# Optimization experiments

Hardware: AMD Instinct MI355X
Metric: run time of the kernel (lower is better)

The kernel has to match this reference:

```python
import jax, jax.numpy as jnp
import numpy as np

EPS = 1e-5


def setup_inputs() -> dict:
    key = jax.random.key(0)
    ks = jax.random.split(key, 8)
    g, p, d, h, w = 32, 64, 512, 24, 8
    hw = h * w
    return {
        "gal_fea": jax.random.normal(ks[0], (g, d, h, w), dtype=jnp.float32),
        "prob_fea": jax.random.normal(ks[1], (p, d, h, w), dtype=jnp.float32),
        "bn_weight": jnp.ones((1,), jnp.float32),
        "bn_bias": jnp.zeros((1,), jnp.float32),
        "bn_mean": jax.random.normal(ks[2], (1,), jnp.float32) * 0.1,
        "bn_var": jax.random.uniform(ks[3], (1,), jnp.float32, 0.5, 1.5),
        "fc_weight": jax.random.normal(ks[4], (1, 2 * hw), jnp.float32) * 0.05,
        "fc_bias": jnp.zeros((1,), jnp.float32),
        "lbn_weight": jnp.ones((1,), jnp.float32),
        "lbn_bias": jnp.zeros((1,), jnp.float32),
        "lbn_mean": jax.random.normal(ks[5], (1,), jnp.float32) * 0.1,
        "lbn_var": jax.random.uniform(ks[6], (1,), jnp.float32, 0.5, 1.5),
    }


def reference(gal_fea, prob_fea, bn_weight, bn_bias, bn_mean, bn_var,
              fc_weight, fc_bias, lbn_weight, lbn_bias, lbn_mean, lbn_var):
    g, d, h, w = gal_fea.shape
    p = prob_fea.shape[0]
    hw = h * w
    # 1x1 conv with probe pixels as kernels == batched correlation (QK^T style)
    gal = gal_fea.reshape(g, d, hw)                                  # [g, d, hw_x]
    ker = jnp.transpose(prob_fea, (0, 2, 3, 1)).reshape(p, hw, d)    # [p, hw_y, d]
    s = jnp.einsum('gdx,pyd->gpyx', gal, ker)                        # [g, p, hw_y, hw_x]
    # dual-axis max pooling, then concat: [g, p, 2*hw]
    score = jnp.concatenate([s.max(axis=2), s.max(axis=3)], axis=-1)
    # BatchNorm1d(1) in eval mode: scalar affine with running stats
    score = (score - bn_mean) * (bn_weight / jnp.sqrt(bn_var + EPS)) + bn_bias
    # fc: Linear(2*hw, 1)
    score = score.reshape(g * p, 2 * hw) @ fc_weight[0] + fc_bias[0]  # [g*p]
    score = score.reshape(g, p)
    # logit BatchNorm1d(1), eval mode
    score = (score - lbn_mean) * (lbn_weight / jnp.sqrt(lbn_var + EPS)) + lbn_bias
    return jax.nn.sigmoid(score / 10.0)
```

## Files before the change

kernel.cpp:

```cpp
#include <hip/hip_runtime.h>
#include <hip/hip_bf16.h>
#include <cstdint>
#include <cstddef>

#define NG 32
#define NP 64
#define ND 512
#define HW 192
#define KS 32
#define EPSV 1e-5f

typedef _Float16 half8 __attribute__((ext_vector_type(8)));
typedef float floatx4 __attribute__((ext_vector_type(4)));
typedef float floatx16 __attribute__((ext_vector_type(16)));

__global__ __launch_bounds__(256) void prep_frag(const float* __restrict__ gal,
                                                 const float* __restrict__ prob,
                                                 _Float16* __restrict__ galT4,
                                                 _Float16* __restrict__ probT4) {
  __shared__ float lds[16 * 192];
  const int z = blockIdx.x;
  const int ks = blockIdx.y;
  const float* src;
  _Float16* dst;
  if (z < NP) {
    src = prob + (size_t)z * ND * HW;
    dst = probT4 + (size_t)z * 98304;
  } else {
    src = gal + (size_t)(z - NP) * ND * HW;
    dst = galT4 + (size_t)(z - NP) * 98304;
  }
  src += (size_t)ks * 16 * HW;
  dst += (size_t)ks * 3072;
  const int t = threadIdx.x;
#pragma unroll
  for (int i = 0; i < 12; ++i) lds[i * 256 + t] = src[i * 256 + t];
  __syncthreads();
#pragma unroll
  for (int r = 0; r < 2; ++r) {
    const int h = r * 256 + t;
    if (h < 384) {
      const int rb = h >> 6, hi = (h >> 5) & 1, l31 = h & 31;
      half8 v;
#pragma unroll
      for (int j = 0; j < 8; ++j) v[j] = (_Float16)lds[(hi * 8 + j) * 192 + rb * 32 + l31];
      *(half8*)(dst + (size_t)h * 8) = v;
    }
  }
}

__device__ __forceinline__ void g2l16(const void* g, void* l) {
  __builtin_amdgcn_global_load_lds(
      (const __attribute__((address_space(1))) void*)g,
      (__attribute__((address_space(3))) void*)l, 16, 0, 0);
}

__global__ __launch_bounds__(256, 2) void qaconv_main(
    const _Float16* __restrict__ galT4, const _Float16* __restrict__ probT4,
    const float* __restrict__ bn_w, const float* __restrict__ bn_b,
    const float* __restrict__ bn_m, const float* __restrict__ bn_v,
    const float* __restrict__ fc_w, const float* __restrict__ fc_b,
    const float* __restrict__ lbn_w, const float* __restrict__ lbn_b,
    const float* __restrict__ lbn_m, const float* __restrict__ lbn_v,
    float* __restrict__ out) {
  __shared__ __align__(16) char shmem[73728];
  __shared__ float colp[2][HW];
  __shared__ float wsum[4];
  float(*rowbuf)[66] = (float(*)[66])shmem;

  const int bid = blockIdx.x;
  const int g = bid >> 6, p = bid & 63;

  const int t = threadIdx.x;
  const int lane = t & 63, wid = t >> 6;
  const int wr = wid & 1;
  const int wc = wid >> 1;
  const int l31 = lane & 31, hi = lane >> 5;

  const _Float16* pAl = probT4 + (size_t)p * 98304 + wid * 512 + lane * 8;
  const _Float16* pBl = galT4 + (size_t)g * 98304 + wid * 512 + lane * 8;
  const int sdst = wid * 1024;

  char* const b0 = shmem;
  char* const b1 = shmem + 24576;
  char* const b2 = shmem + 49152;

  floatx16 acc[3][3];
#pragma unroll
  for (int ii = 0; ii < 3; ++ii)
#pragma unroll
    for (int jj = 0; jj < 3; ++jj) acc[ii][jj] = (floatx16)0.f;

  half8 raf[3], rbf[3];

#define STAGE(kt_, base_)                                            \
  {                                                                  \
    char* db_ = (base_) + sdst;                                      \
    const _Float16* sa_ = pAl + (size_t)(kt_)*6144;                  \
    const _Float16* sb_ = pBl + (size_t)(kt_)*6144;                  \
    g2l16(sa_, db_);                                                 \
    g2l16(sa_ + 2048, db_ + 4096);                                   \
    g2l16(sa_ + 4096, db_ + 8192);                                   \
    g2l16(sb_, db_ + 12288);                                         \
    g2l16(sb_ + 2048, db_ + 16384);                                  \
    g2l16(sb_ + 4096, db_ + 20480);                                  \
  }

#define READ6(base_, kc_)                                            \
  {                                                                  \
    const char* bA_ = (base_) + (kc_)*6144;                          \
    const char* bB_ = (base_) + 12288 + (kc_)*6144;                  \
    raf[0] = *(const half8*)(bA_ + (wr * 3 + 0) * 1024 + lane * 16); \
    raf[1] = *(const half8*)(bA_ + (wr * 3 + 1) * 1024 + lane * 16); \
    raf[2] = *(const half8*)(bA_ + (wr * 3 + 2) * 1024 + lane * 16); \
    rbf[0] = *(const half8*)(bB_ + (wc * 3 + 0) * 1024 + lane * 16); \
    rbf[1] = *(const half8*)(bB_ + (wc * 3 + 1) * 1024 + lane * 16); \
    rbf[2] = *(const half8*)(bB_ + (wc * 3 + 2) * 1024 + lane * 16); \
  }

#define MFMA9()                                                                  \
  {                                                                              \
    __builtin_amdgcn_s_setprio(1);                                               \
    _Pragma("unroll") for (int ii = 0; ii < 3; ++ii)                             \
        _Pragma("unroll") for (int jj = 0; jj < 3; ++jj)                         \
            acc[ii][jj] = __builtin_amdgcn_mfma_f32_32x32x16_f16(raf[ii], rbf[jj],\
                                                                 acc[ii][jj], 0, 0, 0); \
    __builtin_amdgcn_s_setprio(0);                                               \
  }

#define SLOT(kt_, rdb_, stb_, doStage_, vmW_)                        \
  {                                                                  \
                                                        \
    READ6(rdb_, 0)                                                   \
    if (doStage_) STAGE((kt_) + 2, stb_)                             \
    __builtin_amdgcn_sched_barrier(0);                               \
    __builtin_amdgcn_s_barrier();                                    \
    asm volatile("s_waitcnt lgkmcnt(0)" ::: "memory");               \
    __builtin_amdgcn_sched_barrier(0);                               \
    MFMA9()                                                          \
    __builtin_amdgcn_s_barrier();                                    \
                                                        \
    READ6(rdb_, 1)                                                   \
    __builtin_amdgcn_sched_barrier(0);                               \
    asm volatile("s_waitcnt vmcnt(" #vmW_ ")" ::: "memory");         \
    __builtin_amdgcn_s_barrier();                                    \
    asm volatile("s_waitcnt lgkmcnt(0)" ::: "memory");               \
    __builtin_amdgcn_sched_barrier(0);                               \
    MFMA9()                                                          \
    __builtin_amdgcn_s_barrier();                                    \
  }

  STAGE(0, b0)
  STAGE(1, b1)
  asm volatile("s_waitcnt vmcnt(6)" ::: "memory");
  __builtin_amdgcn_s_barrier();

#pragma unroll 1
  for (int m = 0; m < 4; ++m) {
    SLOT(3 * m + 0, b0, b2, true, 6)
    SLOT(3 * m + 1, b1, b0, true, 6)
    SLOT(3 * m + 2, b2, b1, true, 6)
  }
  SLOT(12, b0, b2, true, 6)
  SLOT(13, b1, b0, true, 6)
  SLOT(14, b2, b1, false, 0)
  SLOT(15, b0, b1, false, 0)
#undef STAGE
#undef READ6
#undef MFMA9
#undef SLOT

#pragma unroll
  for (int fb = 0; fb < 3; ++fb) {
    float v = -3.4e38f;
#pragma unroll
    for (int fa = 0; fa < 3; ++fa)
#pragma unroll
      for (int e = 0; e < 16; ++e) v = fmaxf(v, acc[fa][fb][e]);
    v = fmaxf(v, __shfl_xor(v, 32));
    if (lane < 32) colp[wr][wc * 96 + fb * 32 + lane] = v;
  }
  __syncthreads();
#pragma unroll
  for (int fa = 0; fa < 3; ++fa)
#pragma unroll
    for (int e = 0; e < 16; ++e) {
      float rv = acc[fa][0][e];
      rv = fmaxf(rv, acc[fa][1][e]);
      rv = fmaxf(rv, acc[fa][2][e]);
      const int Y = wr * 96 + fa * 32 + (e & 3) + 8 * (e >> 2) + 4 * hi;
      rowbuf[Y][wc * 32 + l31] = rv;
    }
  __syncthreads();

  float partial = 0.f;
  if (t < HW) {
    const float* rb = rowbuf[t];
    float rmax = -3.4e38f;
#pragma unroll
    for (int j = 0; j < 16; ++j) {
      const floatx4 v = *(const floatx4*)&rb[j * 4];
      rmax = fmaxf(rmax, fmaxf(fmaxf(v[0], v[1]), fmaxf(v[2], v[3])));
    }
    const float cmax = fmaxf(colp[0][t], colp[1][t]);
    const float scale = bn_w[0] / sqrtf(bn_v[0] + EPSV);
    const float bm = bn_m[0], bb = bn_b[0];
    partial = ((cmax - bm) * scale + bb) * fc_w[t] +
              ((rmax - bm) * scale + bb) * fc_w[HW + t];
  }
#pragma unroll
  for (int off = 1; off < 64; off <<= 1) partial += __shfl_xor(partial, off);
  if (lane == 0) wsum[wid] = partial;
  __syncthreads();
  if (t == 0) {
    const float sum = fc_b[0] + wsum[0] + wsum[1] + wsum[2] + wsum[3];
    const float logit = (sum - lbn_m[0]) * (lbn_w[0] / sqrtf(lbn_v[0] + EPSV)) + lbn_b[0];
    out[bid] = 1.f / (1.f + expf(-logit * 0.1f));
  }
}

__global__ __launch_bounds__(256) void qaconv_naive(
    const float* __restrict__ gal, const float* __restrict__ prob,
    const float* __restrict__ bn_w, const float* __restrict__ bn_b,
    const float* __restrict__ bn_m, const float* __restrict__ bn_v,
    const float* __restrict__ fc_w, const float* __restrict__ fc_b,
    const float* __restrict__ lbn_w, const float* __restrict__ lbn_b,
    const float* __restrict__ lbn_m, const float* __restrict__ lbn_v,
    float* __restrict__ out) {
  __shared__ float prow[ND];
  __shared__ float rowmaxs[HW];
  __shared__ float colmaxs[HW];
  __shared__ float red[4];
  const int bid = blockIdx.x;
  const int g = bid >> 6, p = bid & 63;
  const int t = threadIdx.x, lane = t & 63, wid = t >> 6;
  const float* gp = gal + (size_t)g * ND * HW;
  const float* pp = prob + (size_t)p * ND * HW;
  float colmax = -3.4e38f;
  for (int y = 0; y < HW; ++y) {
    for (int k = t; k < ND; k += 256) prow[k] = pp[(size_t)k * HW + y];
    __syncthreads();
    float sv = -3.4e38f;
    if (t < HW) {
      sv = 0.f;
      for (int k = 0; k < ND; ++k) sv = fmaf(prow[k], gp[(size_t)k * HW + t], sv);
      colmax = fmaxf(colmax, sv);
    }
    float m = sv;
#pragma unroll
    for (int off = 1; off < 64; off <<= 1) m = fmaxf(m, __shfl_xor(m, off));
    if (lane == 0) red[wid] = m;
    __syncthreads();
    if (t == 0) rowmaxs[y] = fmaxf(fmaxf(red[0], red[1]), fmaxf(red[2], red[3]));
    __syncthreads();
  }
  if (t < HW) colmaxs[t] = colmax;
  __syncthreads();
  float partial = 0.f;
  for (int j = t; j < 2 * HW; j += 256) {
    const float v = (j < HW) ? colmaxs[j] : rowmaxs[j - HW];
    const float sc = (v - bn_m[0]) * (bn_w[0] / sqrtf(bn_v[0] + EPSV)) + bn_b[0];
    partial += sc * fc_w[j];
  }
#pragma unroll
  for (int off = 1; off < 64; off <<= 1) partial += __shfl_xor(partial, off);
  if (lane == 0) red[wid] = partial;
  __syncthreads();
  if (t == 0) {
    const float sum = fc_b[0] + red[0] + red[1] + red[2] + red[3];
    const float logit = (sum - lbn_m[0]) * (lbn_w[0] / sqrtf(lbn_v[0] + EPSV)) + lbn_b[0];
    out[bid] = 1.f / (1.f + expf(-logit * 0.1f));
  }
}

extern "C" void kernel_launch(void* const* d_in, const int* in_sizes, int n_in,
                              void* d_out, int out_size, void* d_ws, size_t ws_size,
                              hipStream_t stream) {
  const float* gal = (const float*)d_in[0];
  const float* prob = (const float*)d_in[1];
  const float* bn_w = (const float*)d_in[2];
  const float* bn_b = (const float*)d_in[3];
  const float* bn_m = (const float*)d_in[4];
  const float* bn_v = (const float*)d_in[5];
  const float* fc_w = (const float*)d_in[6];
  const float* fc_b = (const float*)d_in[7];
  const float* lbn_w = (const float*)d_in[8];
  const float* lbn_b = (const float*)d_in[9];
  const float* lbn_m = (const float*)d_in[10];
  const float* lbn_v = (const float*)d_in[11];
  float* out = (float*)d_out;

  const size_t probT4_elems = (size_t)NP * 98304;
  const size_t galT4_elems = (size_t)NG * 98304;
  const size_t ws_needed = (probT4_elems + galT4_elems) * sizeof(_Float16);
  if (ws_size >= ws_needed) {
    _Float16* probT4 = (_Float16*)d_ws;
    _Float16* galT4 = probT4 + probT4_elems;
    prep_frag<<<dim3(NP + NG, KS), dim3(256), 0, stream>>>(gal, prob, galT4, probT4);
    qaconv_main<<<dim3(NG * NP), dim3(256), 0, stream>>>(
        galT4, probT4, bn_w, bn_b, bn_m, bn_v, fc_w, fc_b, lbn_w, lbn_b, lbn_m, lbn_v, out);
  } else {
    qaconv_naive<<<dim3(NG * NP), dim3(256), 0, stream>>>(
        gal, prob, bn_w, bn_b, bn_m, bn_v, fc_w, fc_b, lbn_w, lbn_b, lbn_m, lbn_v, out);
  }
}
```

Measured before the change: 89.88 us.

## Double-buffer MFMA register fragments to overlap LDS reads with matrix math

```diff
diff --git a/kernel.cpp b/kernel.cpp
--- a/kernel.cpp
+++ b/kernel.cpp
@@ -91,7 +91,7 @@
 #pragma unroll
     for (int jj = 0; jj < 3; ++jj) acc[ii][jj] = (floatx16)0.f;
 
-  half8 raf[3], rbf[3];
+  half8 raf0[3], rbf0[3], raf1[3], rbf1[3];
 
 #define STAGE(kt_, base_)                                            \
   {                                                                  \
@@ -106,47 +106,39 @@
     g2l16(sb_ + 4096, db_ + 20480);                                  \
   }
 
-#define READ6(base_, kc_)                                            \
+#define READ6(AF, BF, base_, kc_)                                    \
   {                                                                  \
     const char* bA_ = (base_) + (kc_)*6144;                          \
     const char* bB_ = (base_) + 12288 + (kc_)*6144;                  \
-    raf[0] = *(const half8*)(bA_ + (wr * 3 + 0) * 1024 + lane * 16); \
-    raf[1] = *(const half8*)(bA_ + (wr * 3 + 1) * 1024 + lane * 16); \
-    raf[2] = *(const half8*)(bA_ + (wr * 3 + 2) * 1024 + lane * 16); \
-    rbf[0] = *(const half8*)(bB_ + (wc * 3 + 0) * 1024 + lane * 16); \
-    rbf[1] = *(const half8*)(bB_ + (wc * 3 + 1) * 1024 + lane * 16); \
-    rbf[2] = *(const half8*)(bB_ + (wc * 3 + 2) * 1024 + lane * 16); \
-  }
-
-#define MFMA9()                                                                  \
+    AF[0] = *(const half8*)(bA_ + (wr * 3 + 0) * 1024 + lane * 16);  \
+    AF[1] = *(const half8*)(bA_ + (wr * 3 + 1) * 1024 + lane * 16);  \
+    AF[2] = *(const half8*)(bA_ + (wr * 3 + 2) * 1024 + lane * 16);  \
+    BF[0] = *(const half8*)(bB_ + (wc * 3 + 0) * 1024 + lane * 16);  \
+    BF[1] = *(const half8*)(bB_ + (wc * 3 + 1) * 1024 + lane * 16);  \
+    BF[2] = *(const half8*)(bB_ + (wc * 3 + 2) * 1024 + lane * 16);  \
+  }
+
+#define MFMA9(AF, BF)                                                            \
   {                                                                              \
     __builtin_amdgcn_s_setprio(1);                                               \
     _Pragma("unroll") for (int ii = 0; ii < 3; ++ii)                             \
         _Pragma("unroll") for (int jj = 0; jj < 3; ++jj)                         \
-            acc[ii][jj] = __builtin_amdgcn_mfma_f32_32x32x16_f16(raf[ii], rbf[jj],\
+            acc[ii][jj] = __builtin_amdgcn_mfma_f32_32x32x16_f16(AF[ii], BF[jj], \
                                                                  acc[ii][jj], 0, 0, 0); \
     __builtin_amdgcn_s_setprio(0);                                               \
   }
 
-#define SLOT(kt_, rdb_, stb_, doStage_, vmW_)                        \
+#define SLOT(kt_, rdb_, nrdb_, stb_, doStage_, vmW_)                 \
   {                                                                  \
-                                                        \
-    READ6(rdb_, 0)                                                   \
+         \
     if (doStage_) STAGE((kt_) + 2, stb_)                             \
-    __builtin_amdgcn_sched_barrier(0);                               \
+    READ6(raf1, rbf1, rdb_, 1)                                       \
+    MFMA9(raf0, rbf0)                                                \
     __builtin_amdgcn_s_barrier();                                    \
-    asm volatile("s_waitcnt lgkmcnt(0)" ::: "memory");               \
-    __builtin_amdgcn_sched_barrier(0);                               \
-    MFMA9()                                                          \
-    __builtin_amdgcn_s_barrier();                                    \
-                                                        \
-    READ6(rdb_, 1)                                                   \
-    __builtin_amdgcn_sched_barrier(0);                               \
+                 \
     asm volatile("s_waitcnt vmcnt(" #vmW_ ")" ::: "memory");         \
-    __builtin_amdgcn_s_barrier();                                    \
-    asm volatile("s_waitcnt lgkmcnt(0)" ::: "memory");               \
-    __builtin_amdgcn_sched_barrier(0);                               \
-    MFMA9()                                                          \
+    READ6(raf0, rbf0, nrdb_, 0)                                      \
+    MFMA9(raf1, rbf1)                                                \
     __builtin_amdgcn_s_barrier();                                    \
   }
 
@@ -154,17 +146,20 @@
   STAGE(1, b1)
   asm volatile("s_waitcnt vmcnt(6)" ::: "memory");
   __builtin_amdgcn_s_barrier();
+  READ6(raf0, rbf0, b0, 0)
 
 #pragma unroll 1
   for (int m = 0; m < 4; ++m) {
-    SLOT(3 * m + 0, b0, b2, true, 6)
-    SLOT(3 * m + 1, b1, b0, true, 6)
-    SLOT(3 * m + 2, b2, b1, true, 6)
-  }
-  SLOT(12, b0, b2, true, 6)
-  SLOT(13, b1, b0, true, 6)
-  SLOT(14, b2, b1, false, 0)
-  SLOT(15, b0, b1, false, 0)
+    SLOT(3 * m + 0, b0, b1, b2, true, 6)
+    SLOT(3 * m + 1, b1, b2, b0, true, 6)
+    SLOT(3 * m + 2, b2, b0, b1, true, 6)
+  }
+  SLOT(12, b0, b1, b2, true, 6)
+  SLOT(13, b1, b2, b0, true, 6)
+  SLOT(14, b2, b0, b1, false, 0)
+  READ6(raf1, rbf1, b0, 1)
+  MFMA9(raf0, rbf0)
+  MFMA9(raf1, rbf1)
 #undef STAGE
 #undef READ6
 #undef MFMA9
```

Measured after the change: 91.95 us. 2.3% more time.

## Process four probes per block with pipeline continuing across pairs

Applied to the files above, without the earlier changes.

```diff
diff --git a/kernel.cpp b/kernel.cpp
--- a/kernel.cpp
+++ b/kernel.cpp
@@ -63,13 +63,14 @@
     const float* __restrict__ lbn_w, const float* __restrict__ lbn_b,
     const float* __restrict__ lbn_m, const float* __restrict__ lbn_v,
     float* __restrict__ out) {
-  __shared__ __align__(16) char shmem[73728];
+  __shared__ __align__(16) char tiles[3][24576];
   __shared__ float colp[2][HW];
+  __shared__ float rowp[2][HW];
   __shared__ float wsum[4];
-  float(*rowbuf)[66] = (float(*)[66])shmem;
 
   const int bid = blockIdx.x;
-  const int g = bid >> 6, p = bid & 63;
+  const int g = bid >> 4;
+  const int p0 = (bid & 15) * 4;
 
   const int t = threadIdx.x;
   const int lane = t & 63, wid = t >> 6;
@@ -77,27 +78,30 @@
   const int wc = wid >> 1;
   const int l31 = lane & 31, hi = lane >> 5;
 
-  const _Float16* pAl = probT4 + (size_t)p * 98304 + wid * 512 + lane * 8;
-  const _Float16* pBl = galT4 + (size_t)g * 98304 + wid * 512 + lane * 8;
-  const int sdst = wid * 1024;
-
-  char* const b0 = shmem;
-  char* const b1 = shmem + 24576;
-  char* const b2 = shmem + 49152;
+  const float scale = bn_w[0] / sqrtf(bn_v[0] + EPSV);
+  const float bm = bn_m[0], bb = bn_b[0];
+  const float lscale = lbn_w[0] / sqrtf(lbn_v[0] + EPSV);
+  const float lm = lbn_m[0], lb = lbn_b[0];
+  const float fcb = fc_b[0];
+
+  const _Float16* pB = galT4 + (size_t)g * 98304 + (size_t)t * 8;
+  const _Float16* pA0 = probT4 + (size_t)p0 * 98304 + (size_t)t * 8;
+  const _Float16* pA1 = pA0 + 98304;
+  const _Float16* pA2 = pA1 + 98304;
+  const _Float16* pA3 = pA2 + 98304;
+
+  char* const T0 = tiles[0];
+  char* const T1 = tiles[1];
+  char* const T2 = tiles[2];
 
   floatx16 acc[3][3];
-#pragma unroll
-  for (int ii = 0; ii < 3; ++ii)
-#pragma unroll
-    for (int jj = 0; jj < 3; ++jj) acc[ii][jj] = (floatx16)0.f;
-
   half8 raf[3], rbf[3];
 
-#define STAGE(kt_, base_)                                            \
+#define STAGE(sA_, kt_, base_)                                       \
   {                                                                  \
-    char* db_ = (base_) + sdst;                                      \
-    const _Float16* sa_ = pAl + (size_t)(kt_)*6144;                  \
-    const _Float16* sb_ = pBl + (size_t)(kt_)*6144;                  \
+    char* db_ = (char*)(base_) + t * 16;                             \
+    const _Float16* sa_ = (sA_) + (size_t)(kt_)*6144;                \
+    const _Float16* sb_ = pB + (size_t)(kt_)*6144;                   \
     g2l16(sa_, db_);                                                 \
     g2l16(sa_ + 2048, db_ + 4096);                                   \
     g2l16(sa_ + 4096, db_ + 8192);                                   \
@@ -108,8 +112,8 @@
 
 #define READ6(base_, kc_)                                            \
   {                                                                  \
-    const char* bA_ = (base_) + (kc_)*6144;                          \
-    const char* bB_ = (base_) + 12288 + (kc_)*6144;                  \
+    const char* bA_ = (const char*)(base_) + (kc_)*6144;             \
+    const char* bB_ = (const char*)(base_) + 12288 + (kc_)*6144;     \
     raf[0] = *(const half8*)(bA_ + (wr * 3 + 0) * 1024 + lane * 16); \
     raf[1] = *(const half8*)(bA_ + (wr * 3 + 1) * 1024 + lane * 16); \
     raf[2] = *(const half8*)(bA_ + (wr * 3 + 2) * 1024 + lane * 16); \
@@ -128,95 +132,120 @@
     __builtin_amdgcn_s_setprio(0);                                               \
   }
 
-#define SLOT(kt_, rdb_, stb_, doStage_, vmW_)                        \
-  {                                                                  \
-                                                        \
-    READ6(rdb_, 0)                                                   \
-    if (doStage_) STAGE((kt_) + 2, stb_)                             \
-    __builtin_amdgcn_sched_barrier(0);                               \
-    __builtin_amdgcn_s_barrier();                                    \
-    asm volatile("s_waitcnt lgkmcnt(0)" ::: "memory");               \
-    __builtin_amdgcn_sched_barrier(0);                               \
-    MFMA9()                                                          \
-    __builtin_amdgcn_s_barrier();                                    \
-                                                        \
-    READ6(rdb_, 1)                                                   \
-    __builtin_amdgcn_sched_barrier(0);                               \
-    asm volatile("s_waitcnt vmcnt(" #vmW_ ")" ::: "memory");         \
-    __builtin_amdgcn_s_barrier();                                    \
-    asm volatile("s_waitcnt lgkmcnt(0)" ::: "memory");               \
-    __builtin_amdgcn_sched_barrier(0);                               \
-    MFMA9()                                                          \
-    __builtin_amdgcn_s_barrier();                                    \
-  }
-
-  STAGE(0, b0)
-  STAGE(1, b1)
-  asm volatile("s_waitcnt vmcnt(6)" ::: "memory");
+#define SLOT(rdb_, stb_, sA_, skt_, doStage_, vmW_)          \
+  {                                                          \
+    READ6(rdb_, 0)                                           \
+    if (doStage_) STAGE(sA_, skt_, stb_)                     \
+    __builtin_amdgcn_sched_barrier(0);                       \
+    __builtin_amdgcn_s_barrier();                            \
+    asm volatile("s_waitcnt lgkmcnt(0)" ::: "memory");       \
+    __builtin_amdgcn_sched_barrier(0);                       \
+    MFMA9()                                                  \
+    __builtin_amdgcn_s_barrier();                            \
+    READ6(rdb_, 1)                                           \
+    __builtin_amdgcn_sched_barrier(0);                       \
+    asm volatile("s_waitcnt vmcnt(" #vmW_ ")" ::: "memory"); \
+    __builtin_amdgcn_s_barrier();                            \
+    asm volatile("s_waitcnt lgkmcnt(0)" ::: "memory");       \
+    __builtin_amdgcn_sched_barrier(0);                       \
+    MFMA9()                                                  \
+    __builtin_amdgcn_s_barrier();                            \
+  }
+
+#define EPI(pidx_)                                                               \
+  {                                                                              \
+    _Pragma("unroll") for (int fb = 0; fb < 3; ++fb) {                           \
+      float v = -3.4e38f;                                                        \
+      _Pragma("unroll") for (int fa = 0; fa < 3; ++fa)                           \
+          _Pragma("unroll") for (int e = 0; e < 16; ++e)                         \
+              v = fmaxf(v, acc[fa][fb][e]);                                      \
+      v = fmaxf(v, __shfl_xor(v, 32));                                           \
+      if (lane < 32) colp[wr][wc * 96 + fb * 32 + lane] = v;                     \
+    }                                                                            \
+    _Pragma("unroll") for (int fa = 0; fa < 3; ++fa)                             \
+        _Pragma("unroll") for (int e = 0; e < 16; ++e) {                         \
+      float rv = fmaxf(fmaxf(acc[fa][0][e], acc[fa][1][e]), acc[fa][2][e]);      \
+      rv = fmaxf(rv, __shfl_xor(rv, 1));                                         \
+      rv = fmaxf(rv, __shfl_xor(rv, 2));                                         \
+      rv = fmaxf(rv, __shfl_xor(rv, 4));                                         \
+      rv = fmaxf(rv, __shfl_xor(rv, 8));                                         \
+      rv = fmaxf(rv, __shfl_xor(rv, 16));                                        \
+      if (l31 == 0) {                                                            \
+        const int Y = wr * 96 + fa * 32 + (e & 3) + 8 * (e >> 2) + 4 * hi;       \
+        rowp[wc][Y] = rv;                                                        \
+      }                                                                          \
+    }                                                                            \
+    asm volatile("s_waitcnt lgkmcnt(0)" ::: "memory");                           \
+    __builtin_amdgcn_s_barrier();                                                \
+    float partial = 0.f;                                                         \
+    if (t < HW) {                                                                \
+      const float rmax = fmaxf(rowp[0][t], rowp[1][t]);                          \
+      const float cmax = fmaxf(colp[0][t], colp[1][t]);                          \
+      partial = ((cmax - bm) * scale + bb) * fc_w[t] +                           \
+                ((rmax - bm) * scale + bb) * fc_w[HW + t];                       \
+    }                                                                            \
+    _Pragma("unroll") for (int off = 1; off < 64; off <<= 1)                     \
+        partial += __shfl_xor(partial, off);                                     \
+    if (lane == 0) wsum[wid] = partial;                                          \
+    asm volatile("s_waitcnt lgkmcnt(0)" ::: "memory");                           \
+    __builtin_amdgcn_s_barrier();                                                \
+    if (t == 0) {                                                                \
+      const float sum = fcb + wsum[0] + wsum[1] + wsum[2] + wsum[3];             \
+      const float logit = (sum - lm) * lscale + lb;                              \
+      out[pidx_] = 1.f / (1.f + expf(-logit * 0.1f));                            \
+    }                                                                            \
+  }
+
+#define ZACC()                                         \
+  _Pragma("unroll") for (int ii = 0; ii < 3; ++ii)     \
+      _Pragma("unroll") for (int jj = 0; jj < 3; ++jj) \
+          acc[ii][jj] = (floatx16)0.f;
+
+#define PAIRBODY(X0_, X1_, X2_, curA_, nxtA_, pidx_)   \
+  ZACC()                                               \
+  _Pragma("unroll 1") for (int m = 0; m < 4; ++m) {    \
+    SLOT(X0_, X2_, curA_, 3 * m + 2, 1, 3)             \
+    SLOT(X1_, X0_, curA_, 3 * m + 3, 1, 3)             \
+    SLOT(X2_, X1_, curA_, 3 * m + 4, 1, 3)             \
+  }                                                    \
+  SLOT(X0_, X2_, curA_, 14, 1, 3)                      \
+  SLOT(X1_, X0_, curA_, 15, 1, 3)                      \
+  SLOT(X2_, X1_, nxtA_, 0, 1, 3)                       \
+  SLOT(X0_, X2_, nxtA_, 1, 1, 3)                       \
+  EPI(pidx_)
+
+#define PAIRLAST(X0_, X1_, X2_, curA_, pidx_)          \
+  ZACC()                                               \
+  _Pragma("unroll 1") for (int m = 0; m < 4; ++m) {    \
+    SLOT(X0_, X2_, curA_, 3 * m + 2, 1, 3)             \
+    SLOT(X1_, X0_, curA_, 3 * m + 3, 1, 3)             \
+    SLOT(X2_, X1_, curA_, 3 * m + 4, 1, 3)             \
+  }                                                    \
+  SLOT(X0_, X2_, curA_, 14, 1, 3)                      \
+  SLOT(X1_, X0_, curA_, 15, 1, 3)                      \
+  SLOT(X2_, X1_, curA_, 0, 0, 0)                       \
+  SLOT(X0_, X2_, curA_, 0, 0, 0)                       \
+  EPI(pidx_)
+
+  STAGE(pA0, 0, T0)
+  STAGE(pA0, 1, T1)
+  asm volatile("s_waitcnt vmcnt(3)" ::: "memory");
   __builtin_amdgcn_s_barrier();
 
-#pragma unroll 1
-  for (int m = 0; m < 4; ++m) {
-    SLOT(3 * m + 0, b0, b2, true, 6)
-    SLOT(3 * m + 1, b1, b0, true, 6)
-    SLOT(3 * m + 2, b2, b1, true, 6)
-  }
-  SLOT(12, b0, b2, true, 6)
-  SLOT(13, b1, b0, true, 6)
-  SLOT(14, b2, b1, false, 0)
-  SLOT(15, b0, b1, false, 0)
+  const int pidx0 = bid * 4;
+  PAIRBODY(T0, T1, T2, pA0, pA1, pidx0 + 0)
+  PAIRBODY(T1, T2, T0, pA1, pA2, pidx0 + 1)
+  PAIRBODY(T2, T0, T1, pA2, pA3, pidx0 + 2)
+  PAIRLAST(T0, T1, T2, pA3, pidx0 + 3)
+
 #undef STAGE
 #undef READ6
 #undef MFMA9
 #undef SLOT
-
-#pragma unroll
-  for (int fb = 0; fb < 3; ++fb) {
-    float v = -3.4e38f;
-#pragma unroll
-    for (int fa = 0; fa < 3; ++fa)
-#pragma unroll
-      for (int e = 0; e < 16; ++e) v = fmaxf(v, acc[fa][fb][e]);
-    v = fmaxf(v, __shfl_xor(v, 32));
-    if (lane < 32) colp[wr][wc * 96 + fb * 32 + lane] = v;
-  }
-  __syncthreads();
-#pragma unroll
-  for (int fa = 0; fa < 3; ++fa)
-#pragma unroll
-    for (int e = 0; e < 16; ++e) {
-      float rv = acc[fa][0][e];
-      rv = fmaxf(rv, acc[fa][1][e]);
-      rv = fmaxf(rv, acc[fa][2][e]);
-      const int Y = wr * 96 + fa * 32 + (e & 3) + 8 * (e >> 2) + 4 * hi;
-      rowbuf[Y][wc * 32 + l31] = rv;
-    }
-  __syncthreads();
-
-  float partial = 0.f;
-  if (t < HW) {
-    const float* rb = rowbuf[t];
-    float rmax = -3.4e38f;
-#pragma unroll
-    for (int j = 0; j < 16; ++j) {
-      const floatx4 v = *(const floatx4*)&rb[j * 4];
-      rmax = fmaxf(rmax, fmaxf(fmaxf(v[0], v[1]), fmaxf(v[2], v[3])));
-    }
-    const float cmax = fmaxf(colp[0][t], colp[1][t]);
-    const float scale = bn_w[0] / sqrtf(bn_v[0] + EPSV);
-    const float bm = bn_m[0], bb = bn_b[0];
-    partial = ((cmax - bm) * scale + bb) * fc_w[t] +
-              ((rmax - bm) * scale + bb) * fc_w[HW + t];
-  }
-#pragma unroll
-  for (int off = 1; off < 64; off <<= 1) partial += __shfl_xor(partial, off);
-  if (lane == 0) wsum[wid] = partial;
-  __syncthreads();
-  if (t == 0) {
-    const float sum = fc_b[0] + wsum[0] + wsum[1] + wsum[2] + wsum[3];
-    const float logit = (sum - lbn_m[0]) * (lbn_w[0] / sqrtf(lbn_v[0] + EPSV)) + lbn_b[0];
-    out[bid] = 1.f / (1.f + expf(-logit * 0.1f));
-  }
+#undef EPI
+#undef ZACC
+#undef PAIRBODY
+#undef PAIRLAST
 }
 
 __global__ __launch_bounds__(256) void qaconv_naive(
@@ -297,7 +326,7 @@
     _Float16* probT4 = (_Float16*)d_ws;
     _Float16* galT4 = probT4 + probT4_elems;
     prep_frag<<<dim3(NP + NG, KS), dim3(256), 0, stream>>>(gal, prob, galT4, probT4);
-    qaconv_main<<<dim3(NG * NP), dim3(256), 0, stream>>>(
+    qaconv_main<<<dim3(512), dim3(256), 0, stream>>>(
         galT4, probT4, bn_w, bn_b, bn_m, bn_v, fc_w, fc_b, lbn_w, lbn_b, lbn_m, lbn_v, out);
   } else {
     qaconv_naive<<<dim3(NG * NP), dim3(256), 0, stream>>>(
```

New measurement: 115.1 us. 1.28x slower.

## Load probe A fragments directly from global into registers, stage only gallery in LDS

Applied to the files above, without the earlier changes.

```diff
diff --git a/kernel.cpp b/kernel.cpp
--- a/kernel.cpp
+++ b/kernel.cpp
@@ -63,7 +63,7 @@
     const float* __restrict__ lbn_w, const float* __restrict__ lbn_b,
     const float* __restrict__ lbn_m, const float* __restrict__ lbn_v,
     float* __restrict__ out) {
-  __shared__ __align__(16) char shmem[73728];
+  __shared__ __align__(16) char shmem[50688];
   __shared__ float colp[2][HW];
   __shared__ float wsum[4];
   float(*rowbuf)[66] = (float(*)[66])shmem;
@@ -77,13 +77,13 @@
   const int wc = wid >> 1;
   const int l31 = lane & 31, hi = lane >> 5;
 
-  const _Float16* pAl = probT4 + (size_t)p * 98304 + wid * 512 + lane * 8;
-  const _Float16* pBl = galT4 + (size_t)g * 98304 + wid * 512 + lane * 8;
-  const int sdst = wid * 1024;
-
-  char* const b0 = shmem;
-  char* const b1 = shmem + 24576;
-  char* const b2 = shmem + 49152;
+  const _Float16* pAw =
+      probT4 + (size_t)p * 98304 + (size_t)(wr * 3) * 512 + (size_t)lane * 8;
+  const _Float16* pBs = galT4 + (size_t)g * 98304 + (size_t)t * 8;
+
+  char* const T0 = shmem;
+  char* const T1 = shmem + 12288;
+  char* const T2 = shmem + 24576;
 
   floatx16 acc[3][3];
 #pragma unroll
@@ -91,82 +91,86 @@
 #pragma unroll
     for (int jj = 0; jj < 3; ++jj) acc[ii][jj] = (floatx16)0.f;
 
-  half8 raf[3], rbf[3];
-
-#define STAGE(kt_, base_)                                            \
+  half8 af0[3], af1[3], bf[3];
+
+#define STAGE_B(kt_, base_)                                          \
   {                                                                  \
-    char* db_ = (base_) + sdst;                                      \
-    const _Float16* sa_ = pAl + (size_t)(kt_)*6144;                  \
-    const _Float16* sb_ = pBl + (size_t)(kt_)*6144;                  \
-    g2l16(sa_, db_);                                                 \
-    g2l16(sa_ + 2048, db_ + 4096);                                   \
-    g2l16(sa_ + 4096, db_ + 8192);                                   \
-    g2l16(sb_, db_ + 12288);                                         \
-    g2l16(sb_ + 2048, db_ + 16384);                                  \
-    g2l16(sb_ + 4096, db_ + 20480);                                  \
-  }
-
-#define READ6(base_, kc_)                                            \
+    char* db_ = (char*)(base_) + t * 16;                             \
+    const _Float16* sb_ = pBs + (size_t)(kt_)*6144;                  \
+    g2l16(sb_, db_);                                                 \
+    g2l16(sb_ + 2048, db_ + 4096);                                   \
+    g2l16(sb_ + 4096, db_ + 8192);                                   \
+  }
+
+#define LOAD_A(AF, f_)                                               \
   {                                                                  \
-    const char* bA_ = (base_) + (kc_)*6144;                          \
-    const char* bB_ = (base_) + 12288 + (kc_)*6144;                  \
-    raf[0] = *(const half8*)(bA_ + (wr * 3 + 0) * 1024 + lane * 16); \
-    raf[1] = *(const half8*)(bA_ + (wr * 3 + 1) * 1024 + lane * 16); \
-    raf[2] = *(const half8*)(bA_ + (wr * 3 + 2) * 1024 + lane * 16); \
-    rbf[0] = *(const half8*)(bB_ + (wc * 3 + 0) * 1024 + lane * 16); \
-    rbf[1] = *(const half8*)(bB_ + (wc * 3 + 1) * 1024 + lane * 16); \
-    rbf[2] = *(const half8*)(bB_ + (wc * 3 + 2) * 1024 + lane * 16); \
-  }
-
-#define MFMA9()                                                                  \
+    const _Float16* a_ = pAw + (size_t)(f_)*3072;                    \
+    AF[0] = *(const half8*)(a_);                                     \
+    AF[1] = *(const half8*)(a_ + 512);                               \
+    AF[2] = *(const half8*)(a_ + 1024);                              \
+  }
+
+#define READ_B(base_, kc_)                                           \
+  {                                                                  \
+    const char* bB_ = (const char*)(base_) + (kc_)*6144;             \
+    bf[0] = *(const half8*)(bB_ + (wc * 3 + 0) * 1024 + lane * 16);  \
+    bf[1] = *(const half8*)(bB_ + (wc * 3 + 1) * 1024 + lane * 16);  \
+    bf[2] = *(const half8*)(bB_ + (wc * 3 + 2) * 1024 + lane * 16);  \
+  }
+
+#define MFMA9(AF)                                                                \
   {                                                                              \
     __builtin_amdgcn_s_setprio(1);                                               \
     _Pragma("unroll") for (int ii = 0; ii < 3; ++ii)                             \
         _Pragma("unroll") for (int jj = 0; jj < 3; ++jj)                         \
-            acc[ii][jj] = __builtin_amdgcn_mfma_f32_32x32x16_f16(raf[ii], rbf[jj],\
+            acc[ii][jj] = __builtin_amdgcn_mfma_f32_32x32x16_f16(AF[ii], bf[jj], \
                                                                  acc[ii][jj], 0, 0, 0); \
     __builtin_amdgcn_s_setprio(0);                                               \
   }
 
-#define SLOT(kt_, rdb_, stb_, doStage_, vmW_)                        \
+#define SLOT(kt_, rdb_, stb_, doStage_, doL0_, doL1_, vw0_, vw1_)    \
   {                                                                  \
-                                                        \
-    READ6(rdb_, 0)                                                   \
-    if (doStage_) STAGE((kt_) + 2, stb_)                             \
+    READ_B(rdb_, 0)                                                  \
+    if (doStage_) STAGE_B((kt_) + 2, stb_)                           \
     __builtin_amdgcn_sched_barrier(0);                               \
     __builtin_amdgcn_s_barrier();                                    \
-    asm volatile("s_waitcnt lgkmcnt(0)" ::: "memory");               \
-    __builtin_amdgcn_sched_barrier(0);                               \
-    MFMA9()                                                          \
+    asm volatile("s_waitcnt vmcnt(" #vw0_ ") lgkmcnt(0)" ::: "memory"); \
+    __builtin_amdgcn_sched_barrier(0);                               \
+    MFMA9(af0)                                                       \
+    if (doL0_) LOAD_A(af0, 2 * (kt_) + 2)                            \
+    __builtin_amdgcn_sched_barrier(0);                               \
     __builtin_amdgcn_s_barrier();                                    \
-                                                        \
-    READ6(rdb_, 1)                                                   \
-    __builtin_amdgcn_sched_barrier(0);                               \
-    asm volatile("s_waitcnt vmcnt(" #vmW_ ")" ::: "memory");         \
+    READ_B(rdb_, 1)                                                  \
+    __builtin_amdgcn_sched_barrier(0);                               \
     __builtin_amdgcn_s_barrier();                                    \
-    asm volatile("s_waitcnt lgkmcnt(0)" ::: "memory");               \
-    __builtin_amdgcn_sched_barrier(0);                               \
-    MFMA9()                                                          \
+    asm volatile("s_waitcnt vmcnt(" #vw1_ ") lgkmcnt(0)" ::: "memory"); \
+    __builtin_amdgcn_sched_barrier(0);                               \
+    MFMA9(af1)                                                       \
+    if (doL1_) LOAD_A(af1, 2 * (kt_) + 3)                            \
+    __builtin_amdgcn_sched_barrier(0);                               \
     __builtin_amdgcn_s_barrier();                                    \
   }
 
-  STAGE(0, b0)
-  STAGE(1, b1)
-  asm volatile("s_waitcnt vmcnt(6)" ::: "memory");
+  STAGE_B(0, T0)
+  STAGE_B(1, T1)
+  LOAD_A(af0, 0)
+  LOAD_A(af1, 1)
+  asm volatile("s_waitcnt vmcnt(9)" ::: "memory");
   __builtin_amdgcn_s_barrier();
 
 #pragma unroll 1
   for (int m = 0; m < 4; ++m) {
-    SLOT(3 * m + 0, b0, b2, true, 6)
-    SLOT(3 * m + 1, b1, b0, true, 6)
-    SLOT(3 * m + 2, b2, b1, true, 6)
-  }
-  SLOT(12, b0, b2, true, 6)
-  SLOT(13, b1, b0, true, 6)
-  SLOT(14, b2, b1, false, 0)
-  SLOT(15, b0, b1, false, 0)
-#undef STAGE
-#undef READ6
+    SLOT(3 * m + 0, T0, T2, 1, 1, 1, 6, 6)
+    SLOT(3 * m + 1, T1, T0, 1, 1, 1, 6, 6)
+    SLOT(3 * m + 2, T2, T1, 1, 1, 1, 6, 6)
+  }
+  SLOT(12, T0, T2, 1, 1, 1, 6, 6)
+  SLOT(13, T1, T0, 1, 1, 1, 6, 6)
+  SLOT(14, T2, T1, 0, 1, 1, 3, 3)
+  SLOT(15, T0, T1, 0, 0, 0, 3, 0)
+#undef STAGE_B
+#undef LOAD_A
+#undef READ_B
 #undef MFMA9
 #undef SLOT
 
```

Measured after the change: 92.31 us. +2.7%, slower.
